# Kernel optimization log

Hardware: AMD Instinct MI355X
Metric: run time of the kernel (lower is better)

The kernel has to match this reference:

```python
import jax, jax.numpy as jnp
import numpy as np

N, D, E = 100000, 32, 1600000
EH, NH = 32, 16
TAU = 0.1


def setup_inputs() -> dict:
    key = jax.random.key(0)
    ks = jax.random.split(key, 12)
    x = jax.random.normal(ks[0], (N, D), dtype=jnp.float32)
    edge_index = jax.random.randint(ks[1], (2, E), 0, N, dtype=jnp.int32)
    hsd = jax.random.normal(ks[2], (N,), dtype=jnp.float32)
    s_e1 = 1.0 / np.sqrt(D + 2)
    s_e2 = 1.0 / np.sqrt(EH)
    s_n2 = 1.0 / np.sqrt(NH)
    We1 = jax.random.uniform(ks[3], (D + 2, EH), jnp.float32, -s_e1, s_e1)
    be1 = jax.random.uniform(ks[4], (EH,), jnp.float32, -s_e1, s_e1)
    We2 = jax.random.uniform(ks[5], (EH, 1), jnp.float32, -s_e2, s_e2)
    be2 = jax.random.uniform(ks[6], (1,), jnp.float32, -s_e2, s_e2)
    Wn1 = jax.random.uniform(ks[7], (1, NH), jnp.float32, -1.0, 1.0)
    bn1 = jax.random.uniform(ks[8], (NH,), jnp.float32, -1.0, 1.0)
    Wn2 = jax.random.uniform(ks[9], (NH, 1), jnp.float32, -s_n2, s_n2)
    bn2 = jax.random.uniform(ks[10], (1,), jnp.float32, -s_n2, s_n2)
    return {"x": x, "hsd": hsd, "We1": We1, "be1": be1, "We2": We2, "be2": be2,
            "Wn1": Wn1, "bn1": bn1, "Wn2": Wn2, "bn2": bn2, "edge_index": edge_index}


def reference(x, hsd, We1, be1, We2, be2, Wn1, bn1, Wn2, bn2, edge_index):
    row, col = edge_index[0], edge_index[1]
    n = x.shape[0]
    # normalized HSD (torch.std is unbiased, ddof=1)
    hsd_norm = (hsd - hsd.mean()) / (jnp.std(hsd, ddof=1) + 1e-8)
    # edge MLP input: [hsd_u, hsd_v, |x_u - x_v|]  -> (E, D+2)
    diff_abs = jnp.abs(x[row] - x[col])
    edge_in = jnp.concatenate([hsd_norm[row][:, None], hsd_norm[col][:, None], diff_abs], axis=1)
    h = jax.nn.relu(edge_in @ We1 + be1)
    e_uv = (h @ We2 + be2)[:, 0]  # (E,)
    # segment softmax over destination (col)
    logits = e_uv / TAU
    seg_max = jax.ops.segment_max(logits, col, num_segments=n)
    seg_max = jnp.where(jnp.isfinite(seg_max), seg_max, 0.0)
    ex = jnp.exp(logits - seg_max[col])
    denom = jax.ops.segment_sum(ex, col, num_segments=n)
    alpha_uv = (ex / (denom[col] + 1e-16))[:, None]  # (E,1)
    # node-level gate
    gh = jax.nn.relu(hsd_norm[:, None] @ Wn1 + bn1)
    alpha_bar = jax.nn.sigmoid(gh @ Wn2 + bn2)  # (N,1)
    # degree normalization
    ones = jnp.ones(row.shape[0], dtype=x.dtype)
    src_deg = jnp.sqrt(jnp.clip(jax.ops.segment_sum(ones, row, num_segments=n), 1.0))
    dst_deg = jnp.sqrt(jnp.clip(jax.ops.segment_sum(ones, col, num_segments=n), 1.0))
    edge_w = 1.0 / (src_deg[row] * dst_deg[col])
    low_pass = jax.ops.segment_sum(edge_w[:, None] * x[row], col, num_segments=n)
    high_pass = jax.ops.segment_sum(alpha_uv * (x[col] - x[row]), col, num_segments=n)
    return (1.0 - alpha_bar) * low_pass + alpha_bar * high_pass
```

## Files before the change

### kernel.cpp

```cpp
#include <hip/hip_runtime.h>

#define D_FEAT 32
#define IN_DIM 34
#define EHID 32
#define NHID 16
#define INV_TAU 10.0f
#define SCAN_CHUNK 1024
#define EPB 256
#define XS 36
#define TILE 8192
#define CAP 6144

__device__ __forceinline__ unsigned enc_f32(float f) {
    unsigned b = __float_as_uint(f);
    return (b & 0x80000000u) ? ~b : (b | 0x80000000u);
}
__device__ __forceinline__ float dec_f32(unsigned e) {
    unsigned b = (e & 0x80000000u) ? (e & 0x7fffffffu) : ~e;
    return __uint_as_float(b);
}

__global__ __launch_bounds__(256) void k1_hsd_stats(const float* __restrict__ hsd,
                                                    double* __restrict__ stats, int N) {
    double s = 0.0, s2 = 0.0;
    for (int i = blockIdx.x * 256 + threadIdx.x; i < N; i += gridDim.x * 256) {
        double v = (double)hsd[i];
        s += v; s2 += v * v;
    }
    for (int off = 32; off > 0; off >>= 1) {
        s  += __shfl_down(s,  off, 64);
        s2 += __shfl_down(s2, off, 64);
    }
    __shared__ double ls[4], ls2[4];
    int wid = threadIdx.x >> 6, lid = threadIdx.x & 63;
    if (lid == 0) { ls[wid] = s; ls2[wid] = s2; }
    __syncthreads();
    if (threadIdx.x == 0) {
        double ts = 0.0, t2 = 0.0;
        for (int w = 0; w < 4; ++w) { ts += ls[w]; t2 += ls2[w]; }
        atomicAdd(stats, ts);
        atomicAdd(stats + 1, t2);
    }
}

__global__ __launch_bounds__(256) void k2_node_prep(const float* __restrict__ hsd,
                                                    const double* __restrict__ stats,
                                                    const float* __restrict__ Wn1,
                                                    const float* __restrict__ bn1,
                                                    const float* __restrict__ Wn2,
                                                    const float* __restrict__ bn2,
                                                    float* __restrict__ hsd_norm,
                                                    float* __restrict__ alpha_bar, int N) {
    int n = blockIdx.x * 256 + threadIdx.x;
    if (n >= N) return;
    double sum = stats[0], sumsq = stats[1];
    double mean = sum / (double)N;
    double var  = (sumsq - sum * sum / (double)N) / (double)(N - 1);
    float stdv  = (float)sqrt(var);
    float hn = (hsd[n] - (float)mean) / (stdv + 1e-8f);
    hsd_norm[n] = hn;
    float acc = bn2[0];
#pragma unroll
    for (int k = 0; k < NHID; ++k)
        acc += fmaxf(fmaf(hn, Wn1[k], bn1[k]), 0.0f) * Wn2[k];
    alpha_bar[n] = 1.0f / (1.0f + __expf(-acc));
}

__global__ __launch_bounds__(256) void s1_hist(const int* __restrict__ ei,
                                               int* __restrict__ hist,
                                               int E, int NB, int T, int M) {
    __shared__ int hv[512], hu[512];
    int t = threadIdx.x;
    for (int b = t; b < 512; b += 256) { hv[b] = 0; hu[b] = 0; }
    __syncthreads();
    int base = blockIdx.x * TILE;
    for (int i = t; i < TILE; i += 256) {
        int e = base + i;
        if (e < E) {
            int u = ei[e], v = ei[E + e];
            atomicAdd(&hv[v >> 8], 1);
            atomicAdd(&hu[u >> 8], 1);
        }
    }
    __syncthreads();
    for (int b = t; b < NB; b += 256) {
        hist[b * T + blockIdx.x] = hv[b];
        hist[M + b * T + blockIdx.x] = hu[b];
    }
}

__global__ __launch_bounds__(256) void scan_k1(const int* __restrict__ cnt,
                                               int* __restrict__ out,
                                               int* __restrict__ partials, int N) {
    __shared__ int lds[256];
    int base = blockIdx.x * SCAN_CHUNK;
    int t = threadIdx.x;
    int v[4]; int loc = 0;
#pragma unroll
    for (int k = 0; k < 4; ++k) {
        int idx = base + t * 4 + k;
        v[k] = (idx < N) ? cnt[idx] : 0;
        loc += v[k];
    }
    lds[t] = loc; __syncthreads();
    for (int off = 1; off < 256; off <<= 1) {
        int a = (t >= off) ? lds[t - off] : 0;
        __syncthreads();
        lds[t] += a;
        __syncthreads();
    }
    int run = (t > 0) ? lds[t - 1] : 0;
    if (t == 255) partials[blockIdx.x] = lds[255];
#pragma unroll
    for (int k = 0; k < 4; ++k) {
        run += v[k];
        int idx = base + t * 4 + k;
        if (idx < N) out[idx + 1] = run;
    }
    if (blockIdx.x == 0 && t == 0) out[0] = 0;
}

__global__ __launch_bounds__(256) void scan_k2(int* __restrict__ partials, int B) {
    __shared__ int lds[256];
    int t = threadIdx.x;
    lds[t] = (t < B) ? partials[t] : 0;
    __syncthreads();
    for (int off = 1; off < 256; off <<= 1) {
        int a = (t >= off) ? lds[t - off] : 0;
        __syncthreads();
        lds[t] += a;
        __syncthreads();
    }
    if (t < B) partials[t] = (t > 0) ? lds[t - 1] : 0;
}

__global__ __launch_bounds__(256) void scan_k3(int* __restrict__ out,
                                               const int* __restrict__ partials, int N) {
    int i = blockIdx.x * 256 + threadIdx.x;
    if (i >= N) return;
    out[i + 1] += partials[i / SCAN_CHUNK];
}

__global__ __launch_bounds__(256) void s2_scatter(const int* __restrict__ ei,
                                                  const int* __restrict__ scanAll,
                                                  int2* __restrict__ coarse,
                                                  int* __restrict__ coarseU,
                                                  int E, int NB, int T, int M) {
    __shared__ int curV[512], curU[512];
    int t = threadIdx.x;
    for (int b = t; b < NB; b += 256) {
        curV[b] = scanAll[b * T + blockIdx.x];
        curU[b] = scanAll[M + b * T + blockIdx.x] - E;
    }
    __syncthreads();
    int base = blockIdx.x * TILE;
    for (int i = t; i < TILE; i += 256) {
        int e = base + i;
        if (e < E) {
            int u = ei[e], v = ei[E + e];
            int pv = atomicAdd(&curV[v >> 8], 1);
            coarse[pv] = make_int2(u, v);
            int pu = atomicAdd(&curU[u >> 8], 1);
            coarseU[pu] = u;
        }
    }
}

__global__ __launch_bounds__(256) void s3b_srccnt(const int* __restrict__ coarseU,
                                                  const int* __restrict__ scanAll,
                                                  float* __restrict__ inv_ssrc,
                                                  int N, int E, int NB, int T, int M) {
    __shared__ int cnt[256];
    int t = threadIdx.x;
    int bin = blockIdx.x;
    int start = scanAll[M + bin * T] - E;
    int endv  = scanAll[M + (bin + 1) * T] - E;
    cnt[t] = 0;
    __syncthreads();
    for (int i = start + t; i < endv; i += 256) atomicAdd(&cnt[coarseU[i] & 255], 1);
    __syncthreads();
    int vglob = (bin << 8) + t;
    if (vglob < N) inv_ssrc[vglob] = rsqrtf(fmaxf((float)cnt[t], 1.0f));
}

__global__ __launch_bounds__(256) void k3c_mlp(const float* __restrict__ x,
                                               const float* __restrict__ hsd_norm,
                                               const float* __restrict__ We1,
                                               const float* __restrict__ be1,
                                               const float* __restrict__ We2,
                                               const float* __restrict__ be2,
                                               const int2* __restrict__ esorted,
                                               float* __restrict__ logit, int E) {
    __shared__ float sxu[EPB * XS];
    int t = threadIdx.x;
    int base = blockIdx.x * EPB;

    int q = t & 7;
#pragma unroll
    for (int k = 0; k < 8; ++k) {
        int s = (t >> 3) + 32 * k;
        int e = base + s;
        int u = esorted[(e < E) ? e : (E - 1)].x;
        float4 val = *(const float4*)(x + (size_t)u * D_FEAT + 4 * q);
        *(float4*)(sxu + s * XS + 4 * q) = val;
    }
    __syncthreads();

    int e = base + t;
    if (e >= E) return;
    int2 uv = esorted[e];
    int u = uv.x, v = uv.y;

    float in0 = hsd_norm[u];
    float in1 = hsd_norm[v];

    float diff[D_FEAT];
    const float4* xv = (const float4*)(x + (size_t)v * D_FEAT);
#pragma unroll
    for (int qq = 0; qq < 8; ++qq) {
        float4 a = *(const float4*)(sxu + t * XS + 4 * qq);
        float4 b = xv[qq];
        diff[4 * qq + 0] = fabsf(a.x - b.x);
        diff[4 * qq + 1] = fabsf(a.y - b.y);
        diff[4 * qq + 2] = fabsf(a.z - b.z);
        diff[4 * qq + 3] = fabsf(a.w - b.w);
    }

    float h[EHID];
#pragma unroll
    for (int j = 0; j < EHID; ++j)
        h[j] = fmaf(in0, We1[j], fmaf(in1, We1[EHID + j], be1[j]));
#pragma unroll
    for (int i = 0; i < D_FEAT; ++i) {
        float a = diff[i];
#pragma unroll
        for (int j = 0; j < EHID; ++j)
            h[j] = fmaf(a, We1[(i + 2) * EHID + j], h[j]);
    }
    float acc = be2[0];
#pragma unroll
    for (int j = 0; j < EHID; ++j)
        acc += fmaxf(h[j], 0.0f) * We2[j];

    logit[e] = acc * INV_TAU;
}

__global__ __launch_bounds__(512) void k6a_tab(const int2* __restrict__ coarse,
                                               const float* __restrict__ logit,
                                               const int* __restrict__ scanAll,
                                               const float* __restrict__ inv_ssrc,
                                               const float* __restrict__ alpha_bar,
                                               int* __restrict__ usrc,
                                               float* __restrict__ coefG,
                                               int* __restrict__ dst_off,
                                               float* __restrict__ selfc,
                                               int N, int E, int NB, int T) {
    __shared__ int      su[CAP];
    __shared__ float    slg[CAP];
    __shared__ int      cnt[256];
    __shared__ unsigned mEnc[256];
    __shared__ float    den[256], cA[256], cB[256];
    __shared__ int      base_[256], cur_[256];

    int t = threadIdx.x;
    int bin = blockIdx.x;
    int start = scanAll[bin * T];
    int n = scanAll[(bin + 1) * T] - start;
    if (n > CAP) n = CAP;

    if (t < 256) { cnt[t] = 0; mEnc[t] = 0u; den[t] = 0.0f; }
    __syncthreads();

    for (int i = t; i < n; i += 512) {
        int2 c = coarse[start + i];
        float lgv = logit[start + i];
        int vl = c.y & 255;
        su[i] = c.x | (vl << 17);
        slg[i] = lgv;
        atomicAdd(&cnt[vl], 1);
        atomicMax(&mEnc[vl], enc_f32(lgv));
    }
    __syncthreads();

    for (int i = t; i < n; i += 512) {
        int vl = su[i] >> 17;
        atomicAdd(&den[vl], __expf(slg[i] - dec_f32(mEnc[vl])));
    }
    __syncthreads();

    for (int off = 1; off < 256; off <<= 1) {
        int a = 0;
        if (t < 256 && t >= off) a = cnt[t - off];
        __syncthreads();
        if (t < 256) cnt[t] += a;
        __syncthreads();
    }
    if (t < 256) {
        int b0 = (t > 0) ? cnt[t - 1] : 0;
        base_[t] = b0; cur_[t] = b0;
        int vg = (bin << 8) + t;
        if (vg < N) {
            float ab = alpha_bar[vg];
            float d = den[t];
            float inv_den = 1.0f / (d + 1e-16f);
            int deg = cnt[t] - b0;
            cA[t] = -ab * inv_den;
            cB[t] = (1.0f - ab) * rsqrtf(fmaxf((float)deg, 1.0f));
            dst_off[vg] = start + b0;
            selfc[vg] = ab * (d * inv_den);
        }
    }
    if (bin == 0 && t == 0) dst_off[N] = E;
    __syncthreads();

    for (int i = t; i < n; i += 512) {
        int up = su[i];
        int vl = up >> 17;
        int u = up & 0x1FFFF;
        int p = start + atomicAdd(&cur_[vl], 1);
        float coef = fmaf(cA[vl], __expf(slg[i] - dec_f32(mEnc[vl])), cB[vl] * inv_ssrc[u]);
        usrc[p] = u;
        coefG[p] = coef;
    }
}

__global__ __launch_bounds__(256) void k7_gather(const float* __restrict__ x,
                                                 const int* __restrict__ dst_off,
                                                 const int* __restrict__ usrc,
                                                 const float* __restrict__ coefG,
                                                 const float* __restrict__ selfc,
                                                 float* __restrict__ out, int N) {
    int wid = threadIdx.x >> 6;
    int lane = threadIdx.x & 63;
    int v = blockIdx.x * 4 + wid;
    if (v >= N) return;

    int beg = dst_off[v], end = dst_off[v + 1];
    int half = lane >> 5;
    int l = lane & 31;

    float acc = 0.0f;
    int jj = beg + half;
    for (; jj + 2 < end; jj += 4) {
        int u0 = usrc[jj];
        int u1 = usrc[jj + 2];
        float c0 = coefG[jj];
        float c1 = coefG[jj + 2];
        float x0 = x[(size_t)u0 * D_FEAT + l];
        float x1 = x[(size_t)u1 * D_FEAT + l];
        acc = fmaf(c0, x0, acc);
        acc = fmaf(c1, x1, acc);
    }
    for (; jj < end; jj += 2) {
        int u0 = usrc[jj];
        float c0 = coefG[jj];
        acc = fmaf(c0, x[(size_t)u0 * D_FEAT + l], acc);
    }
    acc += __shfl_xor(acc, 32, 64);

    if (half == 0)
        out[(size_t)v * D_FEAT + l] = fmaf(selfc[v], x[(size_t)v * D_FEAT + l], acc);
}

extern "C" void kernel_launch(void* const* d_in, const int* in_sizes, int n_in,
                              void* d_out, int out_size, void* d_ws, size_t ws_size,
                              hipStream_t stream) {
    const float* x    = (const float*)d_in[0];
    const float* hsd  = (const float*)d_in[1];
    const float* We1  = (const float*)d_in[2];
    const float* be1  = (const float*)d_in[3];
    const float* We2  = (const float*)d_in[4];
    const float* be2  = (const float*)d_in[5];
    const float* Wn1  = (const float*)d_in[6];
    const float* bn1  = (const float*)d_in[7];
    const float* Wn2  = (const float*)d_in[8];
    const float* bn2  = (const float*)d_in[9];
    const int*   ei   = (const int*)d_in[10];
    float* out = (float*)d_out;

    const int N = in_sizes[1];
    const int E = in_sizes[10] / 2;
    const int NB = (N + 255) >> 8;
    const int T  = (E + TILE - 1) / TILE;
    const int M  = NB * T;
    const int M2 = 2 * M;

    char* ws = (char*)d_ws;
    size_t o = 0;
    auto alloc = [&](size_t bytes) { size_t r = o; o += (bytes + 255) & ~(size_t)255; return r; };
    double* stats     = (double*)(ws + alloc(16));
    float*  inv_ssrc  = (float*)(ws + alloc((size_t)4 * N));
    float*  hsd_norm  = (float*)(ws + alloc((size_t)4 * N));
    float*  alpha_bar = (float*)(ws + alloc((size_t)4 * N));
    float*  selfc     = (float*)(ws + alloc((size_t)4 * N));
    int*    dst_off   = (int*)(ws + alloc((size_t)4 * (N + 1)));
    int*    partials  = (int*)(ws + alloc(1024));
    int*    bufH      = (int*)(ws + alloc((size_t)4 * M2));
    int*    bufS      = (int*)(ws + alloc((size_t)4 * (M2 + 1)));
    int2*   coarse    = (int2*)(ws + alloc((size_t)8 * E));
    int*    coarseU   = (int*)(ws + alloc((size_t)4 * E));
    float*  logit     = (float*)coarseU;
    int*    usrc      = (int*)(ws + alloc((size_t)4 * E));
    float*  coefG     = (float*)(ws + alloc((size_t)4 * E));

    hipMemsetAsync(d_ws, 0, 256, stream);

    k1_hsd_stats<<<256, 256, 0, stream>>>(hsd, stats, N);
    k2_node_prep<<<(N + 255) / 256, 256, 0, stream>>>(hsd, stats, Wn1, bn1, Wn2, bn2,
                                                      hsd_norm, alpha_bar, N);

    s1_hist<<<T, 256, 0, stream>>>(ei, bufH, E, NB, T, M);

    int Bs = (M2 + SCAN_CHUNK - 1) / SCAN_CHUNK;
    scan_k1<<<Bs, 256, 0, stream>>>(bufH, bufS, partials, M2);
    scan_k2<<<1, 256, 0, stream>>>(partials, Bs);
    scan_k3<<<(M2 + 255) / 256, 256, 0, stream>>>(bufS, partials, M2);

    s2_scatter<<<T, 256, 0, stream>>>(ei, bufS, coarse, coarseU, E, NB, T, M);
    s3b_srccnt<<<NB, 256, 0, stream>>>(coarseU, bufS, inv_ssrc, N, E, NB, T, M);
    k3c_mlp<<<(E + EPB - 1) / EPB, 256, 0, stream>>>(x, hsd_norm, We1, be1, We2, be2,
                                                     coarse, logit, E);
    k6a_tab<<<NB, 512, 0, stream>>>(coarse, logit, bufS, inv_ssrc, alpha_bar,
                                    usrc, coefG, dst_off, selfc, N, E, NB, T);
    k7_gather<<<(N + 3) / 4, 256, 0, stream>>>(x, dst_off, usrc, coefG, selfc, out, N);
}
```

Baseline: 314.5 us.

## Halve destination bin width, store source features as bf16 in LDS, restructure gather

Destination bins shrink from 256 to 128 nodes, which doubles the number of bins and k6a_tab blocks. The LDS tile drops to CAP 3072, and the scan now handles more partials per thread. In the edge MLP, source feature rows are packed as bf16 in shared memory to cut LDS footprint and raise occupancy, at the cost of precision in the |x_u - x_v| input. The gather kernel now gives each node a 32-lane half-wave with 4-way unrolling instead of a full wave split into two halves plus a shuffle reduction.

```diff
diff --git a/kernel.cpp b/kernel.cpp
--- a/kernel.cpp
+++ b/kernel.cpp
@@ -7,9 +7,12 @@
 #define INV_TAU 10.0f
 #define SCAN_CHUNK 1024
 #define EPB 256
-#define XS 36
+#define XSH 40
 #define TILE 8192
-#define CAP 6144
+#define BSH 7
+#define NBIN 128
+#define BMASK 127
+#define CAP 3072
 
 __device__ __forceinline__ unsigned enc_f32(float f) {
     unsigned b = __float_as_uint(f);
@@ -18,6 +21,11 @@
 __device__ __forceinline__ float dec_f32(unsigned e) {
     unsigned b = (e & 0x80000000u) ? (e & 0x7fffffffu) : ~e;
     return __uint_as_float(b);
+}
+__device__ __forceinline__ unsigned short f2bf(float f) {
+    unsigned u = __float_as_uint(f);
+    u += 0x7fffu + ((u >> 16) & 1u);
+    return (unsigned short)(u >> 16);
 }
 
 __global__ __launch_bounds__(256) void k1_hsd_stats(const float* __restrict__ hsd,
@@ -69,17 +77,17 @@
 __global__ __launch_bounds__(256) void s1_hist(const int* __restrict__ ei,
                                                int* __restrict__ hist,
                                                int E, int NB, int T, int M) {
-    __shared__ int hv[512], hu[512];
-    int t = threadIdx.x;
-    for (int b = t; b < 512; b += 256) { hv[b] = 0; hu[b] = 0; }
+    __shared__ int hv[1024], hu[1024];
+    int t = threadIdx.x;
+    for (int b = t; b < 1024; b += 256) { hv[b] = 0; hu[b] = 0; }
     __syncthreads();
     int base = blockIdx.x * TILE;
     for (int i = t; i < TILE; i += 256) {
         int e = base + i;
         if (e < E) {
             int u = ei[e], v = ei[E + e];
-            atomicAdd(&hv[v >> 8], 1);
-            atomicAdd(&hu[u >> 8], 1);
+            atomicAdd(&hv[v >> BSH], 1);
+            atomicAdd(&hu[u >> BSH], 1);
         }
     }
     __syncthreads();
@@ -123,15 +131,26 @@
 __global__ __launch_bounds__(256) void scan_k2(int* __restrict__ partials, int B) {
     __shared__ int lds[256];
     int t = threadIdx.x;
-    lds[t] = (t < B) ? partials[t] : 0;
-    __syncthreads();
+    int v[4]; int loc = 0;
+#pragma unroll
+    for (int k = 0; k < 4; ++k) {
+        int idx = t * 4 + k;
+        v[k] = (idx < B) ? partials[idx] : 0;
+        loc += v[k];
+    }
+    lds[t] = loc; __syncthreads();
     for (int off = 1; off < 256; off <<= 1) {
         int a = (t >= off) ? lds[t - off] : 0;
         __syncthreads();
         lds[t] += a;
         __syncthreads();
     }
-    if (t < B) partials[t] = (t > 0) ? lds[t - 1] : 0;
+    int run = (t > 0) ? lds[t - 1] : 0;
+#pragma unroll
+    for (int k = 0; k < 4; ++k) {
+        int idx = t * 4 + k;
+        if (idx < B) { partials[idx] = run; run += v[k]; }
+    }
 }
 
 __global__ __launch_bounds__(256) void scan_k3(int* __restrict__ out,
@@ -146,7 +165,7 @@
                                                   int2* __restrict__ coarse,
                                                   int* __restrict__ coarseU,
                                                   int E, int NB, int T, int M) {
-    __shared__ int curV[512], curU[512];
+    __shared__ int curV[1024], curU[1024];
     int t = threadIdx.x;
     for (int b = t; b < NB; b += 256) {
         curV[b] = scanAll[b * T + blockIdx.x];
@@ -158,9 +177,9 @@
         int e = base + i;
         if (e < E) {
             int u = ei[e], v = ei[E + e];
-            int pv = atomicAdd(&curV[v >> 8], 1);
+            int pv = atomicAdd(&curV[v >> BSH], 1);
             coarse[pv] = make_int2(u, v);
-            int pu = atomicAdd(&curU[u >> 8], 1);
+            int pu = atomicAdd(&curU[u >> BSH], 1);
             coarseU[pu] = u;
         }
     }
@@ -170,17 +189,17 @@
                                                   const int* __restrict__ scanAll,
                                                   float* __restrict__ inv_ssrc,
                                                   int N, int E, int NB, int T, int M) {
-    __shared__ int cnt[256];
+    __shared__ int cnt[NBIN];
     int t = threadIdx.x;
     int bin = blockIdx.x;
     int start = scanAll[M + bin * T] - E;
     int endv  = scanAll[M + (bin + 1) * T] - E;
-    cnt[t] = 0;
-    __syncthreads();
-    for (int i = start + t; i < endv; i += 256) atomicAdd(&cnt[coarseU[i] & 255], 1);
-    __syncthreads();
-    int vglob = (bin << 8) + t;
-    if (vglob < N) inv_ssrc[vglob] = rsqrtf(fmaxf((float)cnt[t], 1.0f));
+    if (t < NBIN) cnt[t] = 0;
+    __syncthreads();
+    for (int i = start + t; i < endv; i += 256) atomicAdd(&cnt[coarseU[i] & BMASK], 1);
+    __syncthreads();
+    int vglob = (bin << BSH) + t;
+    if (t < NBIN && vglob < N) inv_ssrc[vglob] = rsqrtf(fmaxf((float)cnt[t], 1.0f));
 }
 
 __global__ __launch_bounds__(256) void k3c_mlp(const float* __restrict__ x,
@@ -191,7 +210,7 @@
                                                const float* __restrict__ be2,
                                                const int2* __restrict__ esorted,
                                                float* __restrict__ logit, int E) {
-    __shared__ float sxu[EPB * XS];
+    __shared__ unsigned short sxu[EPB * XSH];
     int t = threadIdx.x;
     int base = blockIdx.x * EPB;
 
@@ -202,7 +221,10 @@
         int e = base + s;
         int u = esorted[(e < E) ? e : (E - 1)].x;
         float4 val = *(const float4*)(x + (size_t)u * D_FEAT + 4 * q);
-        *(float4*)(sxu + s * XS + 4 * q) = val;
+        ushort4 pk;
+        pk.x = f2bf(val.x); pk.y = f2bf(val.y);
+        pk.z = f2bf(val.z); pk.w = f2bf(val.w);
+        *(ushort4*)(sxu + s * XSH + 4 * q) = pk;
     }
     __syncthreads();
 
@@ -216,14 +238,16 @@
 
     float diff[D_FEAT];
     const float4* xv = (const float4*)(x + (size_t)v * D_FEAT);
+    const unsigned* p = (const unsigned*)(sxu + (size_t)t * XSH);
 #pragma unroll
     for (int qq = 0; qq < 8; ++qq) {
-        float4 a = *(const float4*)(sxu + t * XS + 4 * qq);
         float4 b = xv[qq];
-        diff[4 * qq + 0] = fabsf(a.x - b.x);
-        diff[4 * qq + 1] = fabsf(a.y - b.y);
-        diff[4 * qq + 2] = fabsf(a.z - b.z);
-        diff[4 * qq + 3] = fabsf(a.w - b.w);
+        unsigned ua = p[2 * qq];
+        unsigned ub = p[2 * qq + 1];
+        diff[4 * qq + 0] = fabsf(__uint_as_float(ua << 16) - b.x);
+        diff[4 * qq + 1] = fabsf(__uint_as_float(ua & 0xFFFF0000u) - b.y);
+        diff[4 * qq + 2] = fabsf(__uint_as_float(ub << 16) - b.z);
+        diff[4 * qq + 3] = fabsf(__uint_as_float(ub & 0xFFFF0000u) - b.w);
     }
 
     float h[EHID];
@@ -257,10 +281,10 @@
                                                int N, int E, int NB, int T) {
     __shared__ int      su[CAP];
     __shared__ float    slg[CAP];
-    __shared__ int      cnt[256];
-    __shared__ unsigned mEnc[256];
-    __shared__ float    den[256], cA[256], cB[256];
-    __shared__ int      base_[256], cur_[256];
+    __shared__ int      cnt[NBIN];
+    __shared__ unsigned mEnc[NBIN];
+    __shared__ float    den[NBIN], cA[NBIN], cB[NBIN];
+    __shared__ int      base_[NBIN], cur_[NBIN];
 
     int t = threadIdx.x;
     int bin = blockIdx.x;
@@ -268,13 +292,13 @@
     int n = scanAll[(bin + 1) * T] - start;
     if (n > CAP) n = CAP;
 
-    if (t < 256) { cnt[t] = 0; mEnc[t] = 0u; den[t] = 0.0f; }
+    if (t < NBIN) { cnt[t] = 0; mEnc[t] = 0u; den[t] = 0.0f; }
     __syncthreads();
 
     for (int i = t; i < n; i += 512) {
         int2 c = coarse[start + i];
         float lgv = logit[start + i];
-        int vl = c.y & 255;
+        int vl = c.y & BMASK;
         su[i] = c.x | (vl << 17);
         slg[i] = lgv;
         atomicAdd(&cnt[vl], 1);
@@ -288,17 +312,17 @@
     }
     __syncthreads();
 
-    for (int off = 1; off < 256; off <<= 1) {
+    for (int off = 1; off < NBIN; off <<= 1) {
         int a = 0;
-        if (t < 256 && t >= off) a = cnt[t - off];
-        __syncthreads();
-        if (t < 256) cnt[t] += a;
-        __syncthreads();
-    }
-    if (t < 256) {
+        if (t < NBIN && t >= off) a = cnt[t - off];
+        __syncthreads();
+        if (t < NBIN) cnt[t] += a;
+        __syncthreads();
+    }
+    if (t < NBIN) {
         int b0 = (t > 0) ? cnt[t - 1] : 0;
         base_[t] = b0; cur_[t] = b0;
-        int vg = (bin << 8) + t;
+        int vg = (bin << BSH) + t;
         if (vg < N) {
             float ab = alpha_bar[vg];
             float d = den[t];
@@ -330,36 +354,30 @@
                                                  const float* __restrict__ coefG,
                                                  const float* __restrict__ selfc,
                                                  float* __restrict__ out, int N) {
-    int wid = threadIdx.x >> 6;
-    int lane = threadIdx.x & 63;
-    int v = blockIdx.x * 4 + wid;
+    int v = blockIdx.x * 8 + (threadIdx.x >> 5);
     if (v >= N) return;
+    int l = threadIdx.x & 31;
 
     int beg = dst_off[v], end = dst_off[v + 1];
-    int half = lane >> 5;
-    int l = lane & 31;
 
     float acc = 0.0f;
-    int jj = beg + half;
-    for (; jj + 2 < end; jj += 4) {
-        int u0 = usrc[jj];
-        int u1 = usrc[jj + 2];
-        float c0 = coefG[jj];
-        float c1 = coefG[jj + 2];
+    int j = beg;
+    for (; j + 3 < end; j += 4) {
+        int u0 = usrc[j], u1 = usrc[j + 1], u2 = usrc[j + 2], u3 = usrc[j + 3];
+        float c0 = coefG[j], c1 = coefG[j + 1], c2 = coefG[j + 2], c3 = coefG[j + 3];
         float x0 = x[(size_t)u0 * D_FEAT + l];
         float x1 = x[(size_t)u1 * D_FEAT + l];
+        float x2 = x[(size_t)u2 * D_FEAT + l];
+        float x3 = x[(size_t)u3 * D_FEAT + l];
         acc = fmaf(c0, x0, acc);
         acc = fmaf(c1, x1, acc);
-    }
-    for (; jj < end; jj += 2) {
-        int u0 = usrc[jj];
-        float c0 = coefG[jj];
-        acc = fmaf(c0, x[(size_t)u0 * D_FEAT + l], acc);
-    }
-    acc += __shfl_xor(acc, 32, 64);
-
-    if (half == 0)
-        out[(size_t)v * D_FEAT + l] = fmaf(selfc[v], x[(size_t)v * D_FEAT + l], acc);
+        acc = fmaf(c2, x2, acc);
+        acc = fmaf(c3, x3, acc);
+    }
+    for (; j < end; ++j)
+        acc = fmaf(coefG[j], x[(size_t)usrc[j] * D_FEAT + l], acc);
+
+    out[(size_t)v * D_FEAT + l] = fmaf(selfc[v], x[(size_t)v * D_FEAT + l], acc);
 }
 
 extern "C" void kernel_launch(void* const* d_in, const int* in_sizes, int n_in,
@@ -380,7 +398,7 @@
 
     const int N = in_sizes[1];
     const int E = in_sizes[10] / 2;
-    const int NB = (N + 255) >> 8;
+    const int NB = (N + NBIN - 1) >> BSH;
     const int T  = (E + TILE - 1) / TILE;
     const int M  = NB * T;
     const int M2 = 2 * M;
@@ -394,7 +412,7 @@
     float*  alpha_bar = (float*)(ws + alloc((size_t)4 * N));
     float*  selfc     = (float*)(ws + alloc((size_t)4 * N));
     int*    dst_off   = (int*)(ws + alloc((size_t)4 * (N + 1)));
-    int*    partials  = (int*)(ws + alloc(1024));
+    int*    partials  = (int*)(ws + alloc(4096));
     int*    bufH      = (int*)(ws + alloc((size_t)4 * M2));
     int*    bufS      = (int*)(ws + alloc((size_t)4 * (M2 + 1)));
     int2*   coarse    = (int2*)(ws + alloc((size_t)8 * E));
@@ -422,5 +440,5 @@
                                                      coarse, logit, E);
     k6a_tab<<<NB, 512, 0, stream>>>(coarse, logit, bufS, inv_ssrc, alpha_bar,
                                     usrc, coefG, dst_off, selfc, N, E, NB, T);
-    k7_gather<<<(N + 3) / 4, 256, 0, stream>>>(x, dst_off, usrc, coefG, selfc, out, N);
-}
+    k7_gather<<<(N + 7) / 8, 256, 0, stream>>>(x, dst_off, usrc, coefG, selfc, out, N);
+}
```

Result: faster. 301.6 us (-4.1%).
